# Kernel optimization log

Measured on AMD Instinct MI355X. Metric: run time of the kernel, lower is better.

## Reference

```python
import jax, jax.numpy as jnp
import numpy as np

K = 9          # self.k
DILATION = 1   # self.dilation
L_B = 90       # banded window width (hardcoded in source)


def setup_inputs() -> dict:
    key = jax.random.key(0)
    x = jax.random.normal(key, (4, 64, 8192, 1), dtype=jnp.float32)
    return {"x": x}


def reference(x):
    # F.normalize(x, p=2, dim=1): L2-normalize over the feature (dims) axis
    eps = 1e-12
    norm = jnp.sqrt(jnp.sum(x * x, axis=1, keepdims=True))
    x = x / jnp.maximum(norm, eps)

    # (B, D, N, 1) -> (B, N, D)
    xt = jnp.squeeze(x, -1).transpose(0, 2, 1)
    B, N, D = xt.shape
    kk = K * DILATION  # top-k width used inside dense_knn_matrix

    # pairwise squared distances: |xi|^2 - 2 xi.xj + |xj|^2  -> (B, N, N)
    sq = jnp.sum(xt * xt, axis=-1, keepdims=True)
    dist = sq - 2.0 * jnp.einsum('bnd,bmd->bnm', xt, xt) + sq.transpose(0, 2, 1)

    # band mask: allowed columns j satisfy i - (L_B - 1) <= j <= i
    # (mask_u kills strict upper triangle; mask_d kills cols below the band)
    i = jnp.arange(N)
    allowed = (i[None, :] <= i[:, None]) & (i[None, :] >= i[:, None] - (L_B - 1))
    fmax = jnp.finfo(dist.dtype).max
    dist = jnp.where(allowed[None], dist, fmax)

    # k nearest = top-k of negative distance
    _, nn_idx = jax.lax.top_k(-dist, kk)  # (B, N, kk) int32

    # diagonal neighbor propagation: for row j < L_B, cols > j get row j's
    # nearest-neighbor index (vectorized form of the source's python loop)
    temp = nn_idx[:, :L_B, 0:1]                      # (B, L_B, 1)
    rows = jnp.arange(L_B)[None, :, None]
    cols = jnp.arange(kk)[None, None, :]
    head = jnp.where(cols > rows, temp, nn_idx[:, :L_B])
    nn_idx = jnp.concatenate([head, nn_idx[:, L_B:]], axis=1)

    center = jnp.broadcast_to(i[None, :, None], (B, N, kk)).astype(nn_idx.dtype)
    edge = jnp.stack([nn_idx, center], axis=0)       # (2, B, N, kk)

    # DenseDilated: stride-slice last axis by dilation, then overwrite the
    # first L_B rows with the undilated first K neighbors
    e = edge[:, :, :, ::DILATION]                    # (2, B, N, K)
    e = e.at[:, :, :L_B].set(edge[:, :, :L_B, :K])
    return e
```

## Files before the change

### kernel.cpp

```cpp
#include <hip/hip_runtime.h>
#include <hip/hip_bf16.h>
#include <stdint.h>

#define NPTS 8192
#define DIM  64
#define NB   4
#define KK   9
#define BQ   64
#define RROWS 160
#define SD2  72
#define UD2  91

typedef short bf16x8 __attribute__((ext_vector_type(8)));
typedef float f32x4  __attribute__((ext_vector_type(4)));

__global__ __launch_bounds__(512, 4) void knn_fused(const float* __restrict__ x,
                                                    int* __restrict__ out) {
    __shared__ uint32_t ud[BQ * UD2];
    __shared__ ushort   sb[RROWS * SD2];
    __shared__ float    rnArr[RROWS];

    float2* psumA = (float2*)ud;
    float2* psumB = (float2*)ud + 512;

    const int tid = threadIdx.x;
    const int blk = blockIdx.x;
    const int L   = (blk & 7) * 64 + (blk >> 3);
    const int b   = L >> 7;
    const int n0  = (L & 127) << 6;
    const int gbase = n0 - 90;

    const float* xb = x + (size_t)b * DIM * NPTS;

    const int w = tid >> 6;
    const int l = tid & 63;

    {
        const int g2 = l * 2;
        const int gg = gbase + g2;
        const int gs = (gg < 0) ? 0 : gg;
        const float* src = xb + gs;
        float s0 = 0.f, s1 = 0.f;
        uint32_t pkA[4], pkB[4];
#pragma unroll
        for (int e = 0; e < 4; ++e) {
            const int d = 8 * w + 2 * e;
            float2 v = *reinterpret_cast<const float2*>(&src[(size_t)d * NPTS]);
            float2 u = *reinterpret_cast<const float2*>(&src[(size_t)(d + 1) * NPTS]);
            s0 += v.x * v.x + u.x * u.x;
            s1 += v.y * v.y + u.y * u.y;
            __hip_bfloat162 hA = __float22bfloat162_rn(make_float2(v.x, u.x));
            __hip_bfloat162 hB = __float22bfloat162_rn(make_float2(v.y, u.y));
            pkA[e] = *reinterpret_cast<uint32_t*>(&hA);
            pkB[e] = *reinterpret_cast<uint32_t*>(&hB);
        }
        *reinterpret_cast<uint4*>(&sb[(size_t)g2 * SD2 + 8 * w]) =
            make_uint4(pkA[0], pkA[1], pkA[2], pkA[3]);
        *reinterpret_cast<uint4*>(&sb[(size_t)(g2 + 1) * SD2 + 8 * w]) =
            make_uint4(pkB[0], pkB[1], pkB[2], pkB[3]);
        psumA[tid] = make_float2(s0, s1);
    }
    {
        const int g2 = 128 + (l & 15) * 2;
        const int c  = (w << 2) | (l >> 4);
        const int gg = gbase + g2;
        const int gs = (gg > NPTS - 2) ? (NPTS - 2) : gg;
        const float* src = xb + gs;
        float2 v = *reinterpret_cast<const float2*>(&src[(size_t)(2 * c) * NPTS]);
        float2 u = *reinterpret_cast<const float2*>(&src[(size_t)(2 * c + 1) * NPTS]);
        float s0 = v.x * v.x + u.x * u.x;
        float s1 = v.y * v.y + u.y * u.y;
        __hip_bfloat162 hA = __float22bfloat162_rn(make_float2(v.x, u.x));
        __hip_bfloat162 hB = __float22bfloat162_rn(make_float2(v.y, u.y));
        *reinterpret_cast<uint32_t*>(&sb[(size_t)g2 * SD2 + 2 * c]) =
            *reinterpret_cast<uint32_t*>(&hA);
        *reinterpret_cast<uint32_t*>(&sb[(size_t)(g2 + 1) * SD2 + 2 * c]) =
            *reinterpret_cast<uint32_t*>(&hB);
        s0 += __shfl_xor(s0, 16); s0 += __shfl_xor(s0, 32);
        s1 += __shfl_xor(s1, 16); s1 += __shfl_xor(s1, 32);
        if (l < 16) psumB[w * 16 + l] = make_float2(s0, s1);
    }
    __syncthreads();

    const int qt = w >> 1;
    const int h  = w & 1;
    const int lr = l & 15;
    const int lk = l >> 4;
    const int nrt = 4 - h;

    const ushort* ap = &sb[(size_t)(90 + qt * 16 + lr) * SD2 + lk * 8];
    bf16x8 a0 = *reinterpret_cast<const bf16x8*>(ap);
    bf16x8 a1 = *reinterpret_cast<const bf16x8*>(ap + 32);

    if (tid < 128) {
        const int gp = tid >> 1, comp = tid & 1;
        float s = 0.f;
#pragma unroll
        for (int k = 0; k < 8; ++k)
            s += reinterpret_cast<const float*>(&psumA[k * 64 + gp])[comp];
        rnArr[tid] = 1.0f / fmaxf(sqrtf(s), 1e-12f);
    } else if (tid < 160) {
        const int rr = tid - 128;
        const int gp = rr >> 1, comp = rr & 1;
        float s = 0.f;
#pragma unroll
        for (int k = 0; k < 8; ++k)
            s += reinterpret_cast<const float*>(&psumB[k * 16 + gp])[comp];
        rnArr[tid] = 1.0f / fmaxf(sqrtf(s), 1e-12f);
    }
    __syncthreads();

    {
        float rq[4];
#pragma unroll
        for (int j = 0; j < 4; ++j) rq[j] = rnArr[90 + qt * 16 + lk * 4 + j];
        const int q0 = qt * 16 + lk * 4;
#pragma unroll
        for (int i = 0; i < 4; ++i) {
            if (i < nrt) {
                const int rto = h * 4 + i;
                const int rbase = qt * 16 + rto * 16;
                const ushort* bp = &sb[(size_t)(rbase + lr) * SD2 + lk * 8];
                bf16x8 b0 = *reinterpret_cast<const bf16x8*>(bp);
                bf16x8 b1 = *reinterpret_cast<const bf16x8*>(bp + 32);
                f32x4 acc = {0.f, 0.f, 0.f, 0.f};
                acc = __builtin_amdgcn_mfma_f32_16x16x32_bf16(a0, b0, acc, 0, 0, 0);
                acc = __builtin_amdgcn_mfma_f32_16x16x32_bf16(a1, b1, acc, 0, 0, 0);
                const int r = rbase + lr;
                const float rnr = rnArr[r];
#pragma unroll
                for (int j = 0; j < 4; ++j) {
                    int rel = r - (q0 + j) - 1;
                    if (rel >= 0 && rel <= 89) {
                        float p = acc[j] * rq[j] * rnr;
                        float dist = 2.0f - 2.0f * p;
                        uint32_t uu = __float_as_uint(dist);
                        uu = (uu & 0x80000000u) ? ~uu : (uu | 0x80000000u);
                        ud[(q0 + j) * UD2 + rel] = (uu & 0xFFFFFF80u) | (uint32_t)rel;
                    }
                }
            }
        }
    }
    __syncthreads();

    {
        const int ql = l >> 3;
        const int s  = l & 7;
        const int q  = (w << 3) | ql;
        const int n  = n0 + q;

        uint32_t key[12];
#pragma unroll
        for (int t = 0; t < 12; ++t) {
            int wofs = s + 8 * t;
            int m = n - 89 + wofs;
            bool ok = (wofs <= 89) && (m >= 0);
            uint32_t raw = ud[q * UD2 + (ok ? wofs : 0)];
            key[t] = ok ? raw : 0xFFFFFFFFu;
        }

        uint32_t prev = 0;
        int omKeep = n;
        int om8 = n;
#pragma unroll
        for (int j = 0; j < KK; ++j) {
            uint32_t mn = 0xFFFFFFFFu;
#pragma unroll
            for (int t = 0; t < 12; ++t) {
                uint32_t cand = (key[t] > prev) ? key[t] : 0xFFFFFFFFu;
                mn = (cand < mn) ? cand : mn;
            }
            uint32_t o;
            o = (uint32_t)__shfl_xor((int)mn, 1); mn = (o < mn) ? o : mn;
            o = (uint32_t)__shfl_xor((int)mn, 2); mn = (o < mn) ? o : mn;
            o = (uint32_t)__shfl_xor((int)mn, 4); mn = (o < mn) ? o : mn;
            int om = (mn == 0xFFFFFFFFu) ? n : (n - 89 + (int)(mn & 127u));
            if (j < 8) {
                if (s == j) omKeep = om;
            } else {
                om8 = om;
            }
            prev = mn;
        }

        const int base0 = (b * NPTS + n) * KK;
        const int base1 = NB * NPTS * KK + base0;
        out[base0 + s] = omKeep;
        out[base1 + s] = n;
        if (s == 0) {
            out[base0 + 8] = om8;
            out[base1 + 8] = n;
        }
    }
}

extern "C" void kernel_launch(void* const* d_in, const int* in_sizes, int n_in,
                              void* d_out, int out_size, void* d_ws, size_t ws_size,
                              hipStream_t stream) {
    const float* x = (const float*)d_in[0];
    int* out = (int*)d_out;
    knn_fused<<<NB * (NPTS / BQ), 512, 0, stream>>>(x, out);
}
```

Measured before the change: 13.31 us.

## Process two query tiles per block, reusing the halo and prefetching the second tile

Each block now handles 128 queries as two 64-query tiles, so the 90-row halo is loaded once and shared across both tiles instead of being reloaded per 64 queries. Global loads for the second tile's extra rows are issued before the first tile's MFMA and top-k phase, so their latency overlaps that compute. The grid is halved and launch bounds drop to 2 blocks per CU. The cost is fewer blocks (256 on a large GPU), more shared memory and registers, and serial work within each block.

New measurement: 15.61 us. 17.3% more time.

```diff
diff --git a/kernel.cpp b/kernel.cpp
--- a/kernel.cpp
+++ b/kernel.cpp
@@ -6,28 +6,29 @@
 #define DIM  64
 #define NB   4
 #define KK   9
-#define BQ   64
-#define RROWS 160
+#define TQ   64
+#define NT   2
+#define RROWS 224
 #define SD2  72
 #define UD2  91
 
 typedef short bf16x8 __attribute__((ext_vector_type(8)));
 typedef float f32x4  __attribute__((ext_vector_type(4)));
 
-__global__ __launch_bounds__(512, 4) void knn_fused(const float* __restrict__ x,
+__global__ __launch_bounds__(512, 2) void knn_fused(const float* __restrict__ x,
                                                     int* __restrict__ out) {
-    __shared__ uint32_t ud[BQ * UD2];
     __shared__ ushort   sb[RROWS * SD2];
+    __shared__ uint32_t ud[TQ * UD2];
     __shared__ float    rnArr[RROWS];
-
-    float2* psumA = (float2*)ud;
-    float2* psumB = (float2*)ud + 512;
+    __shared__ float2   psA[512];
+    __shared__ float2   psB[128];
+    __shared__ float2   psC[256];
 
     const int tid = threadIdx.x;
     const int blk = blockIdx.x;
-    const int L   = (blk & 7) * 64 + (blk >> 3);
-    const int b   = L >> 7;
-    const int n0  = (L & 127) << 6;
+    const int L   = (blk & 7) * 32 + (blk >> 3);
+    const int b   = L >> 6;
+    const int n0  = (L & 63) << 7;
     const int gbase = n0 - 90;
 
     const float* xb = x + (size_t)b * DIM * NPTS;
@@ -58,7 +59,7 @@
             make_uint4(pkA[0], pkA[1], pkA[2], pkA[3]);
         *reinterpret_cast<uint4*>(&sb[(size_t)(g2 + 1) * SD2 + 8 * w]) =
             make_uint4(pkB[0], pkB[1], pkB[2], pkB[3]);
-        psumA[tid] = make_float2(s0, s1);
+        psA[tid] = make_float2(s0, s1);
     }
     {
         const int g2 = 128 + (l & 15) * 2;
@@ -78,7 +79,7 @@
             *reinterpret_cast<uint32_t*>(&hB);
         s0 += __shfl_xor(s0, 16); s0 += __shfl_xor(s0, 32);
         s1 += __shfl_xor(s1, 16); s1 += __shfl_xor(s1, 32);
-        if (l < 16) psumB[w * 16 + l] = make_float2(s0, s1);
+        if (l < 16) psB[w * 16 + l] = make_float2(s0, s1);
     }
     __syncthreads();
 
@@ -87,17 +88,18 @@
     const int lr = l & 15;
     const int lk = l >> 4;
     const int nrt = 4 - h;
-
-    const ushort* ap = &sb[(size_t)(90 + qt * 16 + lr) * SD2 + lk * 8];
-    bf16x8 a0 = *reinterpret_cast<const bf16x8*>(ap);
-    bf16x8 a1 = *reinterpret_cast<const bf16x8*>(ap + 32);
+    const int q0 = qt * 16 + lk * 4;
+
+    const ushort* ap1 = &sb[(size_t)(90 + qt * 16 + lr) * SD2 + lk * 8];
+    bf16x8 a0 = *reinterpret_cast<const bf16x8*>(ap1);
+    bf16x8 a1 = *reinterpret_cast<const bf16x8*>(ap1 + 32);
 
     if (tid < 128) {
         const int gp = tid >> 1, comp = tid & 1;
         float s = 0.f;
 #pragma unroll
         for (int k = 0; k < 8; ++k)
-            s += reinterpret_cast<const float*>(&psumA[k * 64 + gp])[comp];
+            s += reinterpret_cast<const float*>(&psA[k * 64 + gp])[comp];
         rnArr[tid] = 1.0f / fmaxf(sqrtf(s), 1e-12f);
     } else if (tid < 160) {
         const int rr = tid - 128;
@@ -105,16 +107,32 @@
         float s = 0.f;
 #pragma unroll
         for (int k = 0; k < 8; ++k)
-            s += reinterpret_cast<const float*>(&psumB[k * 16 + gp])[comp];
+            s += reinterpret_cast<const float*>(&psB[k * 16 + gp])[comp];
         rnArr[tid] = 1.0f / fmaxf(sqrtf(s), 1e-12f);
     }
     __syncthreads();
 
+    float2 t2v[4], t2u[4];
+    const bool t2act = (l < 32);
+    {
+        const int g2 = 160 + 2 * (l & 31);
+        int gg = gbase + g2;
+        int gs = (gg > NPTS - 2) ? (NPTS - 2) : gg;
+        const float* src = xb + gs;
+#pragma unroll
+        for (int e = 0; e < 4; ++e) {
+            const int d = 8 * w + 2 * e;
+            if (t2act) {
+                t2v[e] = *reinterpret_cast<const float2*>(&src[(size_t)d * NPTS]);
+                t2u[e] = *reinterpret_cast<const float2*>(&src[(size_t)(d + 1) * NPTS]);
+            }
+        }
+    }
+
     {
         float rq[4];
 #pragma unroll
-        for (int j = 0; j < 4; ++j) rq[j] = rnArr[90 + qt * 16 + lk * 4 + j];
-        const int q0 = qt * 16 + lk * 4;
+        for (int j = 0; j < 4; ++j) rq[j] = rnArr[90 + q0 + j];
 #pragma unroll
         for (int i = 0; i < 4; ++i) {
             if (i < nrt) {
@@ -193,6 +211,125 @@
             out[base1 + 8] = n;
         }
     }
+
+    if (t2act) {
+        const int g2 = 160 + 2 * (l & 31);
+        float s0 = 0.f, s1 = 0.f;
+        uint32_t pkA[4], pkB[4];
+#pragma unroll
+        for (int e = 0; e < 4; ++e) {
+            float2 v = t2v[e], u = t2u[e];
+            s0 += v.x * v.x + u.x * u.x;
+            s1 += v.y * v.y + u.y * u.y;
+            __hip_bfloat162 hA = __float22bfloat162_rn(make_float2(v.x, u.x));
+            __hip_bfloat162 hB = __float22bfloat162_rn(make_float2(v.y, u.y));
+            pkA[e] = *reinterpret_cast<uint32_t*>(&hA);
+            pkB[e] = *reinterpret_cast<uint32_t*>(&hB);
+        }
+        *reinterpret_cast<uint4*>(&sb[(size_t)g2 * SD2 + 8 * w]) =
+            make_uint4(pkA[0], pkA[1], pkA[2], pkA[3]);
+        *reinterpret_cast<uint4*>(&sb[(size_t)(g2 + 1) * SD2 + 8 * w]) =
+            make_uint4(pkB[0], pkB[1], pkB[2], pkB[3]);
+        psC[w * 32 + (l & 31)] = make_float2(s0, s1);
+    }
+    __syncthreads();
+
+    const ushort* ap2 = &sb[(size_t)(154 + qt * 16 + lr) * SD2 + lk * 8];
+    bf16x8 c0 = *reinterpret_cast<const bf16x8*>(ap2);
+    bf16x8 c1 = *reinterpret_cast<const bf16x8*>(ap2 + 32);
+
+    if (tid < 64) {
+        const int gp = tid >> 1, comp = tid & 1;
+        float s = 0.f;
+#pragma unroll
+        for (int k = 0; k < 8; ++k)
+            s += reinterpret_cast<const float*>(&psC[k * 32 + gp])[comp];
+        rnArr[160 + tid] = 1.0f / fmaxf(sqrtf(s), 1e-12f);
+    }
+    __syncthreads();
+
+    {
+        float rq[4];
+#pragma unroll
+        for (int j = 0; j < 4; ++j) rq[j] = rnArr[154 + q0 + j];
+#pragma unroll
+        for (int i = 0; i < 4; ++i) {
+            if (i < nrt) {
+                const int rto = h * 4 + i;
+                const int rbase = 64 + qt * 16 + rto * 16;
+                const ushort* bp = &sb[(size_t)(rbase + lr) * SD2 + lk * 8];
+                bf16x8 b0 = *reinterpret_cast<const bf16x8*>(bp);
+                bf16x8 b1 = *reinterpret_cast<const bf16x8*>(bp + 32);
+                f32x4 acc = {0.f, 0.f, 0.f, 0.f};
+                acc = __builtin_amdgcn_mfma_f32_16x16x32_bf16(c0, b0, acc, 0, 0, 0);
+                acc = __builtin_amdgcn_mfma_f32_16x16x32_bf16(c1, b1, acc, 0, 0, 0);
+                const int r = rbase + lr;
+                const float rnr = rnArr[r];
+#pragma unroll
+                for (int j = 0; j < 4; ++j) {
+                    int rel = r - 64 - (q0 + j) - 1;
+                    if (rel >= 0 && rel <= 89) {
+                        float p = acc[j] * rq[j] * rnr;
+                        float dist = 2.0f - 2.0f * p;
+                        uint32_t uu = __float_as_uint(dist);
+                        uu = (uu & 0x80000000u) ? ~uu : (uu | 0x80000000u);
+                        ud[(q0 + j) * UD2 + rel] = (uu & 0xFFFFFF80u) | (uint32_t)rel;
+                    }
+                }
+            }
+        }
+    }
+    __syncthreads();
+
+    {
+        const int ql = l >> 3;
+        const int s  = l & 7;
+        const int q  = (w << 3) | ql;
+        const int n  = n0 + 64 + q;
+
+        uint32_t key[12];
+#pragma unroll
+        for (int t = 0; t < 12; ++t) {
+            int wofs = s + 8 * t;
+            int m = n - 89 + wofs;
+            bool ok = (wofs <= 89) && (m >= 0);
+            uint32_t raw = ud[q * UD2 + (ok ? wofs : 0)];
+            key[t] = ok ? raw : 0xFFFFFFFFu;
+        }
+
+        uint32_t prev = 0;
+        int omKeep = n;
+        int om8 = n;
+#pragma unroll
+        for (int j = 0; j < KK; ++j) {
+            uint32_t mn = 0xFFFFFFFFu;
+#pragma unroll
+            for (int t = 0; t < 12; ++t) {
+                uint32_t cand = (key[t] > prev) ? key[t] : 0xFFFFFFFFu;
+                mn = (cand < mn) ? cand : mn;
+            }
+            uint32_t o;
+            o = (uint32_t)__shfl_xor((int)mn, 1); mn = (o < mn) ? o : mn;
+            o = (uint32_t)__shfl_xor((int)mn, 2); mn = (o < mn) ? o : mn;
+            o = (uint32_t)__shfl_xor((int)mn, 4); mn = (o < mn) ? o : mn;
+            int om = (mn == 0xFFFFFFFFu) ? n : (n - 89 + (int)(mn & 127u));
+            if (j < 8) {
+                if (s == j) omKeep = om;
+            } else {
+                om8 = om;
+            }
+            prev = mn;
+        }
+
+        const int base0 = (b * NPTS + n) * KK;
+        const int base1 = NB * NPTS * KK + base0;
+        out[base0 + s] = omKeep;
+        out[base1 + s] = n;
+        if (s == 0) {
+            out[base0 + 8] = om8;
+            out[base1 + 8] = n;
+        }
+    }
 }
 
 extern "C" void kernel_launch(void* const* d_in, const int* in_sizes, int n_in,
@@ -200,5 +337,5 @@
                               hipStream_t stream) {
     const float* x = (const float*)d_in[0];
     int* out = (int*)d_out;
-    knn_fused<<<NB * (NPTS / BQ), 512, 0, stream>>>(x, out);
+    knn_fused<<<NB * (NPTS / (TQ * NT)), 512, 0, stream>>>(x, out);
 }
```

## Halve query tile to 32 rows with 256-thread blocks and simplified staging

Applied to the files above, without the earlier changes.

Shrinks each block from 64 to 32 query points, uses 256 threads and 128 staged rows instead of 160, and doubles the grid to 1024 blocks. The load phase now uses a single uniform pass per thread covering 16 dims, which removes the separate tail-row path and its shuffle reduction. The aim is more blocks and better occupancy and balance across CUs. The cost is that the 90-row halo is now amortized over fewer queries, so redundant global loads and MFMA work per query rise.

New measurement: 13.92 us. +4.6%, slower.

```diff
diff --git a/kernel.cpp b/kernel.cpp
--- a/kernel.cpp
+++ b/kernel.cpp
@@ -6,28 +6,26 @@
 #define DIM  64
 #define NB   4
 #define KK   9
-#define BQ   64
-#define RROWS 160
+#define BQ   32
+#define RROWS 128
 #define SD2  72
 #define UD2  91
 
 typedef short bf16x8 __attribute__((ext_vector_type(8)));
 typedef float f32x4  __attribute__((ext_vector_type(4)));
 
-__global__ __launch_bounds__(512, 4) void knn_fused(const float* __restrict__ x,
+__global__ __launch_bounds__(256, 4) void knn_fused(const float* __restrict__ x,
                                                     int* __restrict__ out) {
+    __shared__ ushort   sb[RROWS * SD2];
     __shared__ uint32_t ud[BQ * UD2];
-    __shared__ ushort   sb[RROWS * SD2];
+    __shared__ float2   psA[256];
     __shared__ float    rnArr[RROWS];
-
-    float2* psumA = (float2*)ud;
-    float2* psumB = (float2*)ud + 512;
 
     const int tid = threadIdx.x;
     const int blk = blockIdx.x;
-    const int L   = (blk & 7) * 64 + (blk >> 3);
-    const int b   = L >> 7;
-    const int n0  = (L & 127) << 6;
+    const int L   = (blk & 7) * 128 + (blk >> 3);
+    const int b   = L >> 8;
+    const int n0  = (L & 255) << 5;
     const int gbase = n0 - 90;
 
     const float* xb = x + (size_t)b * DIM * NPTS;
@@ -37,14 +35,14 @@
 
     {
         const int g2 = l * 2;
-        const int gg = gbase + g2;
-        const int gs = (gg < 0) ? 0 : gg;
+        int gg = gbase + g2;
+        int gs = (gg < 0) ? 0 : ((gg > NPTS - 2) ? (NPTS - 2) : gg);
         const float* src = xb + gs;
         float s0 = 0.f, s1 = 0.f;
-        uint32_t pkA[4], pkB[4];
+        uint32_t pkA[8], pkB[8];
 #pragma unroll
-        for (int e = 0; e < 4; ++e) {
-            const int d = 8 * w + 2 * e;
+        for (int e = 0; e < 8; ++e) {
+            const int d = 16 * w + 2 * e;
             float2 v = *reinterpret_cast<const float2*>(&src[(size_t)d * NPTS]);
             float2 u = *reinterpret_cast<const float2*>(&src[(size_t)(d + 1) * NPTS]);
             s0 += v.x * v.x + u.x * u.x;
@@ -54,31 +52,15 @@
             pkA[e] = *reinterpret_cast<uint32_t*>(&hA);
             pkB[e] = *reinterpret_cast<uint32_t*>(&hB);
         }
-        *reinterpret_cast<uint4*>(&sb[(size_t)g2 * SD2 + 8 * w]) =
+        *reinterpret_cast<uint4*>(&sb[(size_t)g2 * SD2 + 16 * w]) =
             make_uint4(pkA[0], pkA[1], pkA[2], pkA[3]);
-        *reinterpret_cast<uint4*>(&sb[(size_t)(g2 + 1) * SD2 + 8 * w]) =
+        *reinterpret_cast<uint4*>(&sb[(size_t)g2 * SD2 + 16 * w + 8]) =
+            make_uint4(pkA[4], pkA[5], pkA[6], pkA[7]);
+        *reinterpret_cast<uint4*>(&sb[(size_t)(g2 + 1) * SD2 + 16 * w]) =
             make_uint4(pkB[0], pkB[1], pkB[2], pkB[3]);
-        psumA[tid] = make_float2(s0, s1);
-    }
-    {
-        const int g2 = 128 + (l & 15) * 2;
-        const int c  = (w << 2) | (l >> 4);
-        const int gg = gbase + g2;
-        const int gs = (gg > NPTS - 2) ? (NPTS - 2) : gg;
-        const float* src = xb + gs;
-        float2 v = *reinterpret_cast<const float2*>(&src[(size_t)(2 * c) * NPTS]);
-        float2 u = *reinterpret_cast<const float2*>(&src[(size_t)(2 * c + 1) * NPTS]);
-        float s0 = v.x * v.x + u.x * u.x;
-        float s1 = v.y * v.y + u.y * u.y;
-        __hip_bfloat162 hA = __float22bfloat162_rn(make_float2(v.x, u.x));
-        __hip_bfloat162 hB = __float22bfloat162_rn(make_float2(v.y, u.y));
-        *reinterpret_cast<uint32_t*>(&sb[(size_t)g2 * SD2 + 2 * c]) =
-            *reinterpret_cast<uint32_t*>(&hA);
-        *reinterpret_cast<uint32_t*>(&sb[(size_t)(g2 + 1) * SD2 + 2 * c]) =
-            *reinterpret_cast<uint32_t*>(&hB);
-        s0 += __shfl_xor(s0, 16); s0 += __shfl_xor(s0, 32);
-        s1 += __shfl_xor(s1, 16); s1 += __shfl_xor(s1, 32);
-        if (l < 16) psumB[w * 16 + l] = make_float2(s0, s1);
+        *reinterpret_cast<uint4*>(&sb[(size_t)(g2 + 1) * SD2 + 16 * w + 8]) =
+            make_uint4(pkB[4], pkB[5], pkB[6], pkB[7]);
+        psA[tid] = make_float2(s0, s1);
     }
     __syncthreads();
 
@@ -87,6 +69,7 @@
     const int lr = l & 15;
     const int lk = l >> 4;
     const int nrt = 4 - h;
+    const int q0 = qt * 16 + lk * 4;
 
     const ushort* ap = &sb[(size_t)(90 + qt * 16 + lr) * SD2 + lk * 8];
     bf16x8 a0 = *reinterpret_cast<const bf16x8*>(ap);
@@ -96,16 +79,8 @@
         const int gp = tid >> 1, comp = tid & 1;
         float s = 0.f;
 #pragma unroll
-        for (int k = 0; k < 8; ++k)
-            s += reinterpret_cast<const float*>(&psumA[k * 64 + gp])[comp];
-        rnArr[tid] = 1.0f / fmaxf(sqrtf(s), 1e-12f);
-    } else if (tid < 160) {
-        const int rr = tid - 128;
-        const int gp = rr >> 1, comp = rr & 1;
-        float s = 0.f;
-#pragma unroll
-        for (int k = 0; k < 8; ++k)
-            s += reinterpret_cast<const float*>(&psumB[k * 16 + gp])[comp];
+        for (int k = 0; k < 4; ++k)
+            s += reinterpret_cast<const float*>(&psA[k * 64 + gp])[comp];
         rnArr[tid] = 1.0f / fmaxf(sqrtf(s), 1e-12f);
     }
     __syncthreads();
@@ -113,8 +88,7 @@
     {
         float rq[4];
 #pragma unroll
-        for (int j = 0; j < 4; ++j) rq[j] = rnArr[90 + qt * 16 + lk * 4 + j];
-        const int q0 = qt * 16 + lk * 4;
+        for (int j = 0; j < 4; ++j) rq[j] = rnArr[90 + q0 + j];
 #pragma unroll
         for (int i = 0; i < 4; ++i) {
             if (i < nrt) {
@@ -200,5 +174,5 @@
                               hipStream_t stream) {
     const float* x = (const float*)d_in[0];
     int* out = (int*)d_out;
-    knn_fused<<<NB * (NPTS / BQ), 512, 0, stream>>>(x, out);
+    knn_fused<<<NB * (NPTS / BQ), 256, 0, stream>>>(x, out);
 }
```
